# Performance work log

Measured on AMD Instinct MI355X. Metric: run time of the kernel, lower is better.

Reference implementation:

```python
import jax, jax.numpy as jnp
import numpy as np

IMG_SIZE = 416
STRIDES = (8, 16, 32)
OBJ_W = 1.0
BOX_W = 5.0
EPS = 1e-7


def bbox_ciou(b1, b2):
    # b1, b2: [..., 4] in xyxy. Returns CIoU *loss* (1 - CIoU), standard YOLOv5 form.
    b1x1, b1y1, b1x2, b1y2 = b1[..., 0], b1[..., 1], b1[..., 2], b1[..., 3]
    b2x1, b2y1, b2x2, b2y2 = b2[..., 0], b2[..., 1], b2[..., 2], b2[..., 3]
    w1, h1 = b1x2 - b1x1, b1y2 - b1y1
    w2, h2 = b2x2 - b2x1, b2y2 - b2y1
    inter = (jnp.clip(jnp.minimum(b1x2, b2x2) - jnp.maximum(b1x1, b2x1), 0.0)
             * jnp.clip(jnp.minimum(b1y2, b2y2) - jnp.maximum(b1y1, b2y1), 0.0))
    union = w1 * h1 + w2 * h2 - inter + EPS
    iou = inter / union
    cw = jnp.maximum(b1x2, b2x2) - jnp.minimum(b1x1, b2x1)  # enclosing box
    ch = jnp.maximum(b1y2, b2y2) - jnp.minimum(b1y1, b2y1)
    c2 = cw * cw + ch * ch + EPS
    rho2 = ((b2x1 + b2x2 - b1x1 - b1x2) ** 2 + (b2y1 + b2y2 - b1y1 - b1y2) ** 2) / 4.0
    v = (4.0 / (jnp.pi ** 2)) * (jnp.arctan(w2 / (h2 + EPS)) - jnp.arctan(w1 / (h1 + EPS))) ** 2
    alpha = jax.lax.stop_gradient(v / (v - iou + 1.0 + EPS))
    return 1.0 - iou + rho2 / c2 + alpha * v


def _per_image(pred_b, gt_b, H, W, stride):
    # pred_b: [5, H, W]; gt_b: [N, 4] (cx, cy, w, h) normalized to [0,1]
    N = gt_b.shape[0]
    S = IMG_SIZE / stride
    gx = gt_b[:, 0] * S
    gy = gt_b[:, 1] * S
    col = jnp.clip(gx.astype(jnp.int32), 0, W - 1)
    row = jnp.clip(gy.astype(jnp.int32), 0, H - 1)
    off_x = gx - col.astype(gx.dtype)
    off_y = gy - row.astype(gy.dtype)
    # multi-positive: center cell + nearest x-neighbor + nearest y-neighbor
    col_n = jnp.where(off_x < 0.5, col - 1, col + 1)
    vx = jnp.where(off_x < 0.5, col > 0, col < W - 1)
    row_n = jnp.where(off_y < 0.5, row - 1, row + 1)
    vy = jnp.where(off_y < 0.5, row > 0, row < H - 1)
    rows = jnp.concatenate([row, row, row_n])
    cols = jnp.concatenate([col, col_n, col])
    valid = jnp.concatenate([jnp.ones((N,), bool), vx, vy])
    gi = jnp.tile(jnp.arange(N, dtype=jnp.int32), 3)
    flat = jnp.where(valid, rows * W + cols, 0)
    gi_w = jnp.where(valid, gi, -1)
    gt_idx = jnp.full((H * W,), -1, jnp.int32).at[flat].max(gi_w)
    pos = gt_idx >= 0
    gmap = jnp.maximum(gt_idx, 0)

    l = pred_b.reshape(5, -1)  # [5, HW]
    cell = jnp.arange(H * W)
    ccol = (cell % W).astype(pred_b.dtype)
    crow = (cell // W).astype(pred_b.dtype)
    s = stride / IMG_SIZE
    p_cx = (jax.nn.sigmoid(l[1]) * 2.0 - 0.5 + ccol) * s
    p_cy = (jax.nn.sigmoid(l[2]) * 2.0 - 0.5 + crow) * s
    p_w = jnp.exp(jnp.clip(l[3], -5.0, 5.0)) * s
    p_h = jnp.exp(jnp.clip(l[4], -5.0, 5.0)) * s
    t = gt_b[gmap]  # [HW, 4]
    t_cx, t_cy, t_w, t_h = t[:, 0], t[:, 1], t[:, 2], t[:, 3]
    pb = jnp.stack([p_cx - p_w / 2, p_cy - p_h / 2, p_cx + p_w / 2, p_cy + p_h / 2], -1)
    tb = jnp.stack([t_cx - t_w / 2, t_cy - t_h / 2, t_cx + t_w / 2, t_cy + t_h / 2], -1)
    ciou = jnp.maximum(bbox_ciou(pb, tb), 0.0)
    npos = pos.sum()
    box_loss = jnp.where(pos, ciou, 0.0).sum() / jnp.maximum(npos, 1).astype(ciou.dtype)
    # detached IoU objectness targets (torch no_grad block)
    inter = (jnp.clip(jnp.minimum(pb[:, 2], tb[:, 2]) - jnp.maximum(pb[:, 0], tb[:, 0]), 0.0)
             * jnp.clip(jnp.minimum(pb[:, 3], tb[:, 3]) - jnp.maximum(pb[:, 1], tb[:, 1]), 0.0))
    area_p = jnp.maximum(p_w * p_h, EPS)
    area_t = jnp.maximum(t_w * t_h, EPS)
    iou = jnp.clip(inter / (area_p + area_t - inter + EPS), 0.0, 1.0)
    obj_t = jax.lax.stop_gradient(jnp.where(pos, iou, 0.0))
    return l[0], obj_t, box_loss, npos


def _bce_sum(logits, targets):
    return jnp.sum(jnp.maximum(logits, 0.0) - logits * targets
                   + jnp.log1p(jnp.exp(-jnp.abs(logits))))


def _forward(pred0, pred1, pred2, gt):
    total_box = jnp.float32(0.0)
    bce = jnp.float32(0.0)
    total_pos = jnp.int32(0)
    n_items = jnp.int32(0)
    for pred, stride in zip((pred0, pred1, pred2), STRIDES):
        H, W = pred.shape[2], pred.shape[3]
        logits, obj_t, box_l, npos = jax.vmap(
            lambda p, g: _per_image(p, g, H, W, stride))(pred, gt)
        total_box = total_box + box_l.sum()
        n_items = n_items + (npos > 0).sum()
        total_pos = total_pos + npos.sum()
        bce = bce + _bce_sum(logits, obj_t)
    total_obj = bce / jnp.maximum(total_pos.astype(jnp.float32), 1.0)
    total_box = total_box / jnp.maximum(n_items, 1).astype(jnp.float32)
    return OBJ_W * total_obj + BOX_W * total_box


def setup_inputs() -> dict:
    key = jax.random.key(0)
    k0, k1, k2, k3 = jax.random.split(key, 4)
    B, N = 512, 32
    pred0 = jax.random.normal(k0, (B, 5, 52, 52), jnp.float32)
    pred1 = jax.random.normal(k1, (B, 5, 26, 26), jnp.float32)
    pred2 = jax.random.normal(k2, (B, 5, 13, 13), jnp.float32)
    u = jax.random.uniform(k3, (B, N, 4), jnp.float32)
    # cx, cy in [0,1); w, h in [0.02, 0.30)
    gt = jnp.concatenate([u[..., :2], 0.02 + 0.28 * u[..., 2:]], axis=-1)
    return {"pred0": pred0, "pred1": pred1, "pred2": pred2, "gt": gt}


def reference(pred0, pred1, pred2, gt):
    return _forward(pred0, pred1, pred2, gt)
```

## Files before the change

kernel.cpp:

```cpp
#include <hip/hip_runtime.h>
#include <math.h>

#define EPS 1e-7f
#define NB_BCE 512

__device__ __forceinline__ float bce_base(float l) {
    return fmaxf(l, 0.0f) + __logf(1.0f + __expf(-fabsf(l)));
}

__device__ __forceinline__ float sigmoidf_(float x) { return 1.0f / (1.0f + expf(-x)); }

__global__ __launch_bounds__(256) void det_main(
    const float* __restrict__ pred0,
    const float* __restrict__ pred1,
    const float* __restrict__ pred2,
    const float* __restrict__ gt,
    float*       ws_c,
    float4*      ws_pl,
    int B)
{
    __shared__ int   s_map[52 * 52];
    __shared__ float s_redf[4];

    const int tid = threadIdx.x;
    const int bid = blockIdx.x;
    const int nPL = 3 * B;

    if (bid >= nPL) {
        const int cbid = bid - nPL;
        const unsigned E0 = (unsigned)B * 2704u;
        const unsigned E1 = (unsigned)B * 676u;
        const unsigned E2 = (unsigned)B * 169u;
        const unsigned NV4 = (E0 + E1) >> 2;
        float acc = 0.0f;

        for (unsigned v = (unsigned)cbid * 256u + tid; v < NV4; v += NB_BCE * 256u) {
            const unsigned idx = v << 2;
            const float* p;
            if (idx < E0) {
                const unsigned b = idx / 2704u;
                const unsigned i = idx - b * 2704u;
                p = pred0 + (size_t)b * 13520u + i;
            } else {
                const unsigned j = idx - E0;
                const unsigned b = j / 676u;
                const unsigned i = j - b * 676u;
                p = pred1 + (size_t)b * 3380u + i;
            }
            const float4 l = *reinterpret_cast<const float4*>(p);
            acc += bce_base(l.x) + bce_base(l.y) + bce_base(l.z) + bce_base(l.w);
        }
        for (unsigned j = (unsigned)cbid * 256u + tid; j < E2; j += NB_BCE * 256u) {
            const unsigned b = j / 169u;
            const unsigned i = j - b * 169u;
            acc += bce_base(pred2[(size_t)b * 845u + i]);
        }

        for (int off = 32; off > 0; off >>= 1) acc += __shfl_down(acc, off);
        if ((tid & 63) == 0) s_redf[tid >> 6] = acc;
        __syncthreads();
        if (tid == 0) ws_c[cbid] = s_redf[0] + s_redf[1] + s_redf[2] + s_redf[3];
        return;
    }

    if (tid >= 64) return;

    const int pbid  = bid;
    const int level = pbid % 3;
    const int b     = pbid / 3;

    const float* pred;
    int Wd;
    if (level == 0)      { pred = pred0; Wd = 52; }
    else if (level == 1) { pred = pred1; Wd = 26; }
    else                 { pred = pred2; Wd = 13; }
    const int   HW = Wd * Wd;
    const float S  = (float)Wd;
    const float sc = 1.0f / S;

    float box_v = 0.0f, corr_v = 0.0f, np_v = 0.0f;

    if (tid < 32) {
        const int n = tid;
        const float4 g = *reinterpret_cast<const float4*>(gt + (size_t)b * 128 + n * 4);

        const float gx = g.x * S;
        const float gy = g.y * S;
        int col = (int)gx; col = min(max(col, 0), Wd - 1);
        int row = (int)gy; row = min(max(row, 0), Wd - 1);
        const float off_x = gx - (float)col;
        const float off_y = gy - (float)row;

        int col_n, row_n; bool vx, vy;
        if (off_x < 0.5f) { col_n = col - 1; vx = (col > 0); }
        else              { col_n = col + 1; vx = (col < Wd - 1); }
        if (off_y < 0.5f) { row_n = row - 1; vy = (row > 0); }
        else              { row_n = row + 1; vy = (row < Wd - 1); }

        int cs[3];
        cs[0] = row * Wd + col;
        cs[1] = vx ? (row * Wd + col_n) : -1;
        cs[2] = vy ? (row_n * Wd + col) : -1;

        s_map[cs[0]] = -1;
        if (cs[1] >= 0) s_map[cs[1]] = -1;
        if (cs[2] >= 0) s_map[cs[2]] = -1;
        __threadfence_block();
        atomicMax(&s_map[cs[0]], n);
        if (cs[1] >= 0) atomicMax(&s_map[cs[1]], n);
        if (cs[2] >= 0) atomicMax(&s_map[cs[2]], n);
        __threadfence_block();

        const float* base = pred + (size_t)b * 5 * HW;

        const float t_cx = g.x, t_cy = g.y, t_w = g.z, t_h = g.w;
        const float b2x1 = t_cx - t_w * 0.5f, b2y1 = t_cy - t_h * 0.5f;
        const float b2x2 = t_cx + t_w * 0.5f, b2y2 = t_cy + t_h * 0.5f;
        const float w2 = b2x2 - b2x1, h2 = b2y2 - b2y1;
        const float atan2_ = atanf(w2 / (h2 + EPS));
        const float area_t = fmaxf(t_w * t_h, EPS);

        #pragma unroll
        for (int k = 0; k < 3; k++) {
            const int c = cs[k];
            if (c >= 0 && s_map[c] == n) {
                np_v += 1.0f;
                const float l0 = base[c];
                const float l1 = base[HW + c];
                const float l2 = base[2 * HW + c];
                const float l3 = base[3 * HW + c];
                const float l4 = base[4 * HW + c];
                const float ccol = (float)(c % Wd);
                const float crow = (float)(c / Wd);
                const float p_cx = (sigmoidf_(l1) * 2.0f - 0.5f + ccol) * sc;
                const float p_cy = (sigmoidf_(l2) * 2.0f - 0.5f + crow) * sc;
                const float p_w  = expf(fminf(fmaxf(l3, -5.0f), 5.0f)) * sc;
                const float p_h  = expf(fminf(fmaxf(l4, -5.0f), 5.0f)) * sc;

                const float b1x1 = p_cx - p_w * 0.5f, b1y1 = p_cy - p_h * 0.5f;
                const float b1x2 = p_cx + p_w * 0.5f, b1y2 = p_cy + p_h * 0.5f;
                const float w1 = b1x2 - b1x1, h1 = b1y2 - b1y1;

                const float iw = fmaxf(fminf(b1x2, b2x2) - fmaxf(b1x1, b2x1), 0.0f);
                const float ih = fmaxf(fminf(b1y2, b2y2) - fmaxf(b1y1, b2y1), 0.0f);
                const float inter = iw * ih;
                const float uni = w1 * h1 + w2 * h2 - inter + EPS;
                const float iou = inter / uni;

                const float cw = fmaxf(b1x2, b2x2) - fminf(b1x1, b2x1);
                const float ch = fmaxf(b1y2, b2y2) - fminf(b1y1, b2y1);
                const float c2 = cw * cw + ch * ch + EPS;
                const float dx = b2x1 + b2x2 - b1x1 - b1x2;
                const float dy = b2y1 + b2y2 - b1y1 - b1y2;
                const float rho2 = (dx * dx + dy * dy) * 0.25f;
                const float datan = atan2_ - atanf(w1 / (h1 + EPS));
                const float v = (4.0f / (float)(M_PI * M_PI)) * datan * datan;
                const float alpha = v / (v - iou + 1.0f + EPS);
                const float ciou = 1.0f - iou + rho2 / c2 + alpha * v;
                box_v += fmaxf(ciou, 0.0f);

                const float area_p = fmaxf(p_w * p_h, EPS);
                float iou2 = inter / (area_p + area_t - inter + EPS);
                iou2 = fminf(fmaxf(iou2, 0.0f), 1.0f);
                corr_v += l0 * iou2;
            }
        }
    }

    for (int off = 32; off > 0; off >>= 1) {
        box_v  += __shfl_down(box_v, off);
        corr_v += __shfl_down(corr_v, off);
        np_v   += __shfl_down(np_v, off);
    }
    if (tid == 0) {
        const float np = np_v;
        ws_pl[pbid] = make_float4(box_v / fmaxf(np, 1.0f), corr_v, np, (np > 0.0f) ? 1.0f : 0.0f);
    }
}

__global__ __launch_bounds__(256) void det_final(
    const float*  __restrict__ ws_c,
    const float4* __restrict__ ws_pl,
    int nPL,
    float* __restrict__ out)
{
    __shared__ float s_f[20];
    const int tid = threadIdx.x;
    float box = 0.0f, corr = 0.0f, bce = 0.0f, pos = 0.0f, items = 0.0f;
    for (int i = tid; i < nPL; i += 256) {
        const float4 v = ws_pl[i];
        box += v.x; corr += v.y; pos += v.z; items += v.w;
    }
    for (int i = tid; i < NB_BCE; i += 256) bce += ws_c[i];

    for (int off = 32; off > 0; off >>= 1) {
        box   += __shfl_down(box, off);
        corr  += __shfl_down(corr, off);
        bce   += __shfl_down(bce, off);
        pos   += __shfl_down(pos, off);
        items += __shfl_down(items, off);
    }
    const int wave = tid >> 6;
    if ((tid & 63) == 0) {
        s_f[wave * 5 + 0] = box;
        s_f[wave * 5 + 1] = corr;
        s_f[wave * 5 + 2] = bce;
        s_f[wave * 5 + 3] = pos;
        s_f[wave * 5 + 4] = items;
    }
    __syncthreads();
    if (tid == 0) {
        float box_t = 0.0f, corr_t = 0.0f, bce_t = 0.0f, pos_t = 0.0f, it_t = 0.0f;
        for (int w = 0; w < 4; w++) {
            box_t  += s_f[w * 5 + 0];
            corr_t += s_f[w * 5 + 1];
            bce_t  += s_f[w * 5 + 2];
            pos_t  += s_f[w * 5 + 3];
            it_t   += s_f[w * 5 + 4];
        }
        const float total_obj = (bce_t - corr_t) / fmaxf(pos_t, 1.0f);
        const float total_box = box_t / fmaxf(it_t, 1.0f);
        out[0] = total_obj + 5.0f * total_box;
    }
}

extern "C" void kernel_launch(void* const* d_in, const int* in_sizes, int n_in,
                              void* d_out, int out_size, void* d_ws, size_t ws_size,
                              hipStream_t stream)
{
    const float* pred0 = (const float*)d_in[0];
    const float* pred1 = (const float*)d_in[1];
    const float* pred2 = (const float*)d_in[2];
    const float* gt    = (const float*)d_in[3];
    float* out = (float*)d_out;

    const int B   = in_sizes[3] / (32 * 4);
    const int nPL = 3 * B;

    float*  ws_c  = (float*)d_ws;
    float4* ws_pl = (float4*)((char*)d_ws + NB_BCE * sizeof(float));

    det_main<<<dim3(nPL + NB_BCE), dim3(256), 0, stream>>>(
        pred0, pred1, pred2, gt, ws_c, ws_pl, B);
    det_final<<<dim3(1), dim3(256), 0, stream>>>(ws_c, ws_pl, nPL, out);
}
```

Before: 14.95 us.

## Pack four image-level items per block and prefetch logits before scatter

Each 256-thread block now processes four (image, level) items, one per wavefront, each with its own shared-memory cell map, instead of idling three wavefronts. This cuts the positive-path grid from 3B blocks to 3B/4. Candidate-cell logits are loaded from global memory before the shared-memory atomic scatter so load latency overlaps it. Shared memory per block grows fourfold, about 43KB, which can lower occupancy for the BCE blocks running the same kernel. The grid now assumes 3*B is divisible by 4.

```diff
diff --git a/kernel.cpp b/kernel.cpp
--- a/kernel.cpp
+++ b/kernel.cpp
@@ -19,15 +19,16 @@
     float4*      ws_pl,
     int B)
 {
-    __shared__ int   s_map[52 * 52];
+    __shared__ int   s_map[4][52 * 52];
     __shared__ float s_redf[4];
 
     const int tid = threadIdx.x;
     const int bid = blockIdx.x;
-    const int nPL = 3 * B;
-
-    if (bid >= nPL) {
-        const int cbid = bid - nPL;
+    const int nPL   = 3 * B;
+    const int nPosB = nPL >> 2;
+
+    if (bid >= nPosB) {
+        const int cbid = bid - nPosB;
         const unsigned E0 = (unsigned)B * 2704u;
         const unsigned E1 = (unsigned)B * 676u;
         const unsigned E2 = (unsigned)B * 169u;
@@ -63,9 +64,9 @@
         return;
     }
 
-    if (tid >= 64) return;
-
-    const int pbid  = bid;
+    const int wid  = tid >> 6;
+    const int lane = tid & 63;
+    const int pbid = bid * 4 + wid;
     const int level = pbid % 3;
     const int b     = pbid / 3;
 
@@ -78,10 +79,12 @@
     const float S  = (float)Wd;
     const float sc = 1.0f / S;
 
+    int* smap = s_map[wid];
+
     float box_v = 0.0f, corr_v = 0.0f, np_v = 0.0f;
 
-    if (tid < 32) {
-        const int n = tid;
+    if (lane < 32) {
+        const int n = lane;
         const float4 g = *reinterpret_cast<const float4*>(gt + (size_t)b * 128 + n * 4);
 
         const float gx = g.x * S;
@@ -102,16 +105,26 @@
         cs[1] = vx ? (row * Wd + col_n) : -1;
         cs[2] = vy ? (row_n * Wd + col) : -1;
 
-        s_map[cs[0]] = -1;
-        if (cs[1] >= 0) s_map[cs[1]] = -1;
-        if (cs[2] >= 0) s_map[cs[2]] = -1;
+        const float* base = pred + (size_t)b * 5 * HW;
+        float pl0[3], pl1[3], pl2[3], pl3[3], pl4[3];
+        #pragma unroll
+        for (int k = 0; k < 3; k++) {
+            const int cc = (cs[k] >= 0) ? cs[k] : cs[0];
+            pl0[k] = base[cc];
+            pl1[k] = base[HW + cc];
+            pl2[k] = base[2 * HW + cc];
+            pl3[k] = base[3 * HW + cc];
+            pl4[k] = base[4 * HW + cc];
+        }
+
+        smap[cs[0]] = -1;
+        if (cs[1] >= 0) smap[cs[1]] = -1;
+        if (cs[2] >= 0) smap[cs[2]] = -1;
         __threadfence_block();
-        atomicMax(&s_map[cs[0]], n);
-        if (cs[1] >= 0) atomicMax(&s_map[cs[1]], n);
-        if (cs[2] >= 0) atomicMax(&s_map[cs[2]], n);
+        atomicMax(&smap[cs[0]], n);
+        if (cs[1] >= 0) atomicMax(&smap[cs[1]], n);
+        if (cs[2] >= 0) atomicMax(&smap[cs[2]], n);
         __threadfence_block();
-
-        const float* base = pred + (size_t)b * 5 * HW;
 
         const float t_cx = g.x, t_cy = g.y, t_w = g.z, t_h = g.w;
         const float b2x1 = t_cx - t_w * 0.5f, b2y1 = t_cy - t_h * 0.5f;
@@ -123,19 +136,15 @@
         #pragma unroll
         for (int k = 0; k < 3; k++) {
             const int c = cs[k];
-            if (c >= 0 && s_map[c] == n) {
+            if (c >= 0 && smap[c] == n) {
                 np_v += 1.0f;
-                const float l0 = base[c];
-                const float l1 = base[HW + c];
-                const float l2 = base[2 * HW + c];
-                const float l3 = base[3 * HW + c];
-                const float l4 = base[4 * HW + c];
+                const float l0 = pl0[k];
                 const float ccol = (float)(c % Wd);
                 const float crow = (float)(c / Wd);
-                const float p_cx = (sigmoidf_(l1) * 2.0f - 0.5f + ccol) * sc;
-                const float p_cy = (sigmoidf_(l2) * 2.0f - 0.5f + crow) * sc;
-                const float p_w  = expf(fminf(fmaxf(l3, -5.0f), 5.0f)) * sc;
-                const float p_h  = expf(fminf(fmaxf(l4, -5.0f), 5.0f)) * sc;
+                const float p_cx = (sigmoidf_(pl1[k]) * 2.0f - 0.5f + ccol) * sc;
+                const float p_cy = (sigmoidf_(pl2[k]) * 2.0f - 0.5f + crow) * sc;
+                const float p_w  = expf(fminf(fmaxf(pl3[k], -5.0f), 5.0f)) * sc;
+                const float p_h  = expf(fminf(fmaxf(pl4[k], -5.0f), 5.0f)) * sc;
 
                 const float b1x1 = p_cx - p_w * 0.5f, b1y1 = p_cy - p_h * 0.5f;
                 const float b1x2 = p_cx + p_w * 0.5f, b1y2 = p_cy + p_h * 0.5f;
@@ -172,7 +181,7 @@
         corr_v += __shfl_down(corr_v, off);
         np_v   += __shfl_down(np_v, off);
     }
-    if (tid == 0) {
+    if (lane == 0) {
         const float np = np_v;
         ws_pl[pbid] = make_float4(box_v / fmaxf(np, 1.0f), corr_v, np, (np > 0.0f) ? 1.0f : 0.0f);
     }
@@ -240,7 +249,7 @@
     float*  ws_c  = (float*)d_ws;
     float4* ws_pl = (float4*)((char*)d_ws + NB_BCE * sizeof(float));
 
-    det_main<<<dim3(nPL + NB_BCE), dim3(256), 0, stream>>>(
+    det_main<<<dim3(nPL / 4 + NB_BCE), dim3(256), 0, stream>>>(
         pred0, pred1, pred2, gt, ws_c, ws_pl, B);
     det_final<<<dim3(1), dim3(256), 0, stream>>>(ws_c, ws_pl, nPL, out);
 }
```

New measurement: 16.05 us. 7.3% more time.
